# Performance work log

Hardware: AMD Instinct MI355X
Metric: run time of the kernel (lower is better)

The kernel has to match this reference:

```python
import jax, jax.numpy as jnp
import numpy as np
from jax.scipy.ndimage import map_coordinates

N = 512      # image H=W (x0.shape[2])
A = 30       # number of projection angles (sparse-view CT)
D = 729      # det_count (hardcoded in source)
L = 3        # LayerNo
B = 2        # batch
P = 2048     # FFT padding: next pow2 >= 2*D


def _ramp_filter(size):
    # standard Ram-Lak filter built in spatial domain (skimage/torch-radon style)
    n = np.concatenate((np.arange(1, size // 2 + 1, 2), np.arange(size // 2 - 1, 0, -2)))
    f = np.zeros(size)
    f[0] = 0.25
    f[1::2] = -1.0 / (np.pi * n) ** 2
    return jnp.asarray(2.0 * np.real(np.fft.fft(f))[: size // 2 + 1], dtype=jnp.float32)


def setup_inputs() -> dict:
    key = jax.random.key(0)
    ks = jax.random.split(key, 8)
    x0 = jax.random.normal(ks[0], (B, 1, N, N), jnp.float32)
    sinogram = jax.random.normal(ks[1], (B, 1, A, D), jnp.float32)
    theta = jnp.linspace(0.0, np.pi, A, endpoint=False).astype(jnp.float32)
    theta_label = theta
    # denoiser params, stacked over L unrolled layers
    w1 = jax.random.normal(ks[2], (L, 32, 1, 3, 3), jnp.float32) * 0.1
    b1 = jnp.zeros((L, 32), jnp.float32)
    w2 = jax.random.normal(ks[3], (L, 32, 32, 3, 3), jnp.float32) * 0.05
    b2 = jnp.zeros((L, 32), jnp.float32)
    w3 = jax.random.normal(ks[4], (L, 32, 32, 3, 3), jnp.float32) * 0.05
    b3 = jnp.zeros((L, 32), jnp.float32)
    w4 = jax.random.normal(ks[5], (L, 1, 32, 3, 3), jnp.float32) * 0.05
    steps = jnp.ones((L,), jnp.float32)  # step_n params (requires_grad=False)
    return {"cond": 1, "x0": x0, "sinogram": sinogram, "theta": theta,
            "theta_label": theta_label, "w1": w1, "b1": b1, "w2": w2, "b2": b2,
            "w3": w3, "b3": b3, "w4": w4, "steps": steps}


def _conv(x, w, b=None):
    y = jax.lax.conv_general_dilated(x, w, (1, 1), 'SAME',
                                     dimension_numbers=('NCHW', 'OIHW', 'NCHW'))
    return y if b is None else y + b[None, :, None, None]


def _denoiser(x, w1, b1, w2, b2, w3, b3, w4):
    h = jax.nn.relu(_conv(x, w1, b1))
    h = jax.nn.relu(_conv(h, w2, b2))
    h = jax.nn.relu(_conv(h, w3, b3))
    return _conv(h, w4)


def _geometry(theta):
    # parallel-beam ray sampling grid: rows/cols [A, D, T] with T=D samples (dt=1)
    c = (N - 1) / 2.0
    s = jnp.arange(D, dtype=jnp.float32) - (D - 1) / 2.0  # detector coords
    t = s                                                  # along-ray samples
    cs, sn = jnp.cos(theta), jnp.sin(theta)
    x = s[None, :, None] * cs[:, None, None] - t[None, None, :] * sn[:, None, None]
    y = s[None, :, None] * sn[:, None, None] + t[None, None, :] * cs[:, None, None]
    return y + c, x + c  # rows, cols


def _radon_fwd(imgs, rows, cols):
    # imgs [B,N,N] -> sinogram [B,A,D] via bilinear line-integral sampling
    sample = lambda im: map_coordinates(im, [rows, cols], order=1, mode='constant', cval=0.0)
    return jax.vmap(sample)(imgs).sum(-1)


def _filter_sino(sino, filt):
    F = jnp.fft.rfft(sino, n=P, axis=-1)
    g = jnp.fft.irfft(F * filt, n=P, axis=-1)[..., :D]
    return g * (jnp.pi / (2.0 * A))  # FBP normalization


def _backproj(sino, theta):
    # sino [B,A,D] -> image [B,N,N], linear interp along detector axis
    c = (N - 1) / 2.0
    xs = jnp.arange(N, dtype=jnp.float32) - c
    cs, sn = jnp.cos(theta), jnp.sin(theta)
    sgrid = cs[:, None, None] * xs[None, None, :] + sn[:, None, None] * xs[None, :, None]  # [A,N,N]
    idx = sgrid + (D - 1) / 2.0
    lo = jnp.floor(idx).astype(jnp.int32)
    w = idx - lo
    lo_ok = (lo >= 0) & (lo < D)
    hi_ok = (lo + 1 >= 0) & (lo + 1 < D)
    lo_c = jnp.clip(lo, 0, D - 1)
    hi_c = jnp.clip(lo + 1, 0, D - 1)
    a = jnp.arange(A)[:, None, None]
    v = sino[:, a, lo_c] * jnp.where(lo_ok, 1.0 - w, 0.0) + \
        sino[:, a, hi_c] * jnp.where(hi_ok, w, 0.0)       # [B,A,N,N]
    return v.sum(axis=1)


def reference(cond, x0, sinogram, theta, theta_label, w1, b1, w2, b2, w3, b3, w4, steps):
    rows, cols = _geometry(theta)
    filt = _ramp_filter(P)
    X = x0[:, 0]           # [B,N,N]
    sino = sinogram[:, 0]  # [B,A,D]
    for n in range(L):
        sino_pred = _radon_fwd(X, rows, cols)
        filtered = _filter_sino(sino_pred, filt)
        outputs = _backproj(sino - filtered, theta)
        z = X + steps[n] * outputs
        noise = _denoiser(X[:, None], w1[n], b1[n], w2[n], b2[n], w3[n], b3[n], w4[n])[:, 0]
        filtered_noise = _filter_sino(_radon_fwd(noise, rows, cols), filt)
        outputs_noise = _backproj(filtered_noise, theta)
        X = z + noise - steps[n] * outputs_noise
    Xo = X[:, None]
    return (Xo, Xo, Xo)
```

## Files before the change

### kernel.cpp

```cpp
#include <hip/hip_runtime.h>
#include <hip/hip_bf16.h>

typedef __hip_bfloat16 bf16;
typedef __attribute__((ext_vector_type(8))) short short8;
typedef __attribute__((ext_vector_type(4))) short s4v;
typedef __attribute__((ext_vector_type(4))) float float4v;

#define NN 512
#define NA 30
#define ND 729
#define NB 2
#define NL 3
#define BNN (NB*NN*NN)
#define BAD (NB*NA*ND)

#define PW 520
#define PH 516
#define PIMG (PH*PW)
#define POFF (2*PW + 2)

#define O_CS 0
#define O_SN 32
#define O_XP 64
#define O_YP (O_XP + 2*PIMG)
#define O_SP (O_YP + 2*PIMG)
#define O_Q  (O_SP + BAD)
#define O_WR (O_Q + BAD)
#define O_H  (((O_WR + 34560) + 15) & ~15)
#define H_FLOATS (NB * 32 * NN * NN / 2)

#define WR2_OFF 0
#define WR3_OFF 27648
#define WR4_OFF 55296

__global__ void k_prep_all(const float* __restrict__ theta,
                           const float* __restrict__ w2, const float* __restrict__ w3,
                           const float* __restrict__ w4, float* __restrict__ ws,
                           bf16* __restrict__ wr)
{
    int idx = blockIdx.x * 256 + threadIdx.x;
    if (idx < NA) {
        float t = theta[idx];
        ws[O_CS + idx] = cosf(t);
        ws[O_SN + idx] = sinf(t);
    }
    if (idx < 2 * 27648) {
        const float* w = (idx < 27648) ? w2 : w3;
        int base = (idx < 27648) ? WR2_OFF : WR3_OFF;
        int r = idx % 27648;
        int n = r / 9216; int r2 = r % 9216;
        int tap = r2 / 1024; int r3 = r2 % 1024;
        int co = r3 / 32, ci = r3 % 32;
        wr[base + r] = __float2bfloat16(w[n * 9216 + (co * 32 + ci) * 9 + tap]);
    } else if (idx < 2 * 27648 + 3 * 4608) {
        int r = idx - 2 * 27648;
        int n = r / 4608; int r2 = r % 4608;
        int tap = r2 / 512; int r3 = r2 % 512;
        int co = r3 / 32, ci = r3 % 32;
        float v = (co == 0) ? w4[n * 288 + ci * 9 + tap] : 0.f;
        wr[WR4_OFF + r] = __float2bfloat16(v);
    }
}

__global__ void k_init_pad(const float* __restrict__ x0, float* __restrict__ XP,
                           float* __restrict__ YP)
{
    int idx = blockIdx.x * 256 + threadIdx.x;
    if (idx >= 2 * PIMG) return;
    int b = idx / PIMG, p = idx % PIMG;
    int y = p / PW, x = p % PW;
    bool interior = (y >= 2 && y < 2 + NN && x >= 2 && x < 2 + NN);
    float v = interior ? x0[b * NN * NN + (y - 2) * NN + (x - 2)] : 0.f;
    XP[idx] = v;
    if (!interior) YP[idx] = 0.f;
}

__device__ __forceinline__ void isect(float A, float coef, float lo, float hi,
                                      float& tlo, float& thi)
{
    float a = (lo - A) / coef, b = (hi - A) / coef;
    float l = fminf(a, b), h = fmaxf(a, b);
    tlo = fmaxf(tlo, l);
    thi = fminf(thi, h);
}

__global__ __launch_bounds__(256) void k_radon(const float* __restrict__ img,
    const float* __restrict__ ws, float* __restrict__ out)
{
    int b = blockIdx.z, a = blockIdx.y;
    int wave = threadIdx.x >> 6;
    int lane = threadIdx.x & 63;
    int s = blockIdx.x * 4 + wave;
    if (s >= ND) return;
    float cs = ws[O_CS + a], sn = ws[O_SN + a];
    float s_c = (float)s - 364.0f;
    float A_r = 255.5f + s_c * sn;
    float A_c = 255.5f + s_c * cs;

    float tlo = -1e9f, thi = 1e9f;
    isect(A_r, cs, -1.0f, 512.0f, tlo, thi);
    isect(A_c, -sn, -1.0f, 512.0f, tlo, thi);
    float t0f = fmaxf(tlo + 364.0f, 0.0f);
    float t1f = fminf(thi + 364.0f, 728.0f);

    float acc = 0.f;
    if (t0f <= t1f) {
        int tb = (int)ceilf(t0f);
        int te = (int)floorf(t1f);
        const float* im = img + b * PIMG;
#pragma unroll 2
        for (int t = tb + lane; t <= te; t += 64) {
            float tc = (float)t - 364.0f;
            float r = fmaf(tc, cs, A_r);
            float c = fmaf(-tc, sn, A_c);
            float rf = floorf(r), cf = floorf(c);
            float dr = r - rf, dc = c - cf;
            int idx = (int)rf * PW + (int)cf;
            float v00 = im[idx], v01 = im[idx + 1];
            float v10 = im[idx + PW], v11 = im[idx + PW + 1];
            float top = fmaf(dc, v01 - v00, v00);
            float bot = fmaf(dc, v11 - v10, v10);
            acc = fmaf(dr, bot - top, acc + top);
        }
    }
    acc += __shfl_down(acc, 32, 64);
    acc += __shfl_down(acc, 16, 64);
    acc += __shfl_down(acc, 8, 64);
    acc += __shfl_down(acc, 4, 64);
    acc += __shfl_down(acc, 2, 64);
    acc += __shfl_down(acc, 1, 64);
    if (lane == 0) out[(b * NA + a) * ND + s] = acc;
}

__global__ void k_filter(const float* __restrict__ sp, const float* __restrict__ sino,
                         float* __restrict__ q)
{
    __shared__ float row[ND];
    __shared__ float taps[364];
    int ba = blockIdx.y;
    const float* src = sp + ba * ND;
    for (int i = threadIdx.x; i < ND; i += 256) row[i] = src[i];
    const float PI2 = 9.86960440108936f;
    for (int i = threadIdx.x; i < 364; i += 256) {
        float m = (float)(2 * i + 1);
        taps[i] = -2.0f / (PI2 * m * m);
    }
    __syncthreads();
    const float scale = 0.0523598775598299f;
    int d = blockIdx.x * 256 + threadIdx.x;
    if (d < ND) {
        float g0 = 0.5f * row[d], g1 = 0.f;
#pragma unroll 4
        for (int j = 0; j < 364; j += 2) {
            int m0 = 2 * j + 1, m1 = 2 * j + 3;
            float l0 = (d - m0 >= 0) ? row[d - m0] : 0.f;
            float r0 = (d + m0 < ND) ? row[d + m0] : 0.f;
            g0 = fmaf(taps[j], l0 + r0, g0);
            float l1 = (d - m1 >= 0) ? row[d - m1] : 0.f;
            float r1 = (d + m1 < ND) ? row[d + m1] : 0.f;
            g1 = fmaf(taps[j + 1], l1 + r1, g1);
        }
        q[ba * ND + d] = sino[ba * ND + d] - scale * (g0 + g1);
    }
}

__global__ __launch_bounds__(256) void k_backproj_update(const float* __restrict__ q,
    const float* __restrict__ src1, const float* __restrict__ ws,
    const float* __restrict__ steps, int n, float* __restrict__ out,
    float* __restrict__ outcopy)
{
    __shared__ float qt[NA][28];
    __shared__ int dmin_s[NA];
    int b = blockIdx.z;
    int x0 = blockIdx.x * 16, y0 = blockIdx.y * 16;
    int tid = threadIdx.x;
    int lx = tid & 15, ly = tid >> 4;
    const float* qb = q + b * NA * ND;

    for (int idx = tid; idx < NA * 26; idx += 256) {
        int a = idx / 26, j = idx % 26;
        float cs = ws[O_CS + a], sn = ws[O_SN + a];
        float f00 = fmaf(cs, (float)x0 - 255.5f, fmaf(sn, (float)y0 - 255.5f, 364.0f));
        float fmn = f00 + fminf(cs * 15.f, 0.f) + fminf(sn * 15.f, 0.f);
        int dm = (int)floorf(fmn);
        if (j == 0) dmin_s[a] = dm;
        int d = dm + j;
        qt[a][j] = (d >= 0 && d < ND) ? qb[a * ND + d] : 0.f;
    }
    __syncthreads();

    float xc = (float)(x0 + lx) - 255.5f, yc = (float)(y0 + ly) - 255.5f;
    float acc = 0.f;
#pragma unroll
    for (int a = 0; a < NA; a++) {
        float cs = ws[O_CS + a], sn = ws[O_SN + a];
        float f = fmaf(cs, xc, fmaf(sn, yc, 364.0f));
        float lf = floorf(f);
        float w = f - lf;
        int j = (int)lf - dmin_s[a];
        float v0 = qt[a][j], v1 = qt[a][j + 1];
        acc = fmaf(v0, 1.0f - w, fmaf(v1, w, acc));
    }
    int pidx = b * PIMG + (y0 + ly) * PW + (x0 + lx);
    float v = fmaf(steps[n], acc, src1[pidx]);
    out[pidx] = v;
    if (outcopy) {
        int fidx = b * NN * NN + (y0 + ly) * NN + (x0 + lx);
        outcopy[fidx] = v;
        outcopy[fidx + BNN] = v;
        outcopy[fidx + 2 * BNN] = v;
    }
}

__global__ __launch_bounds__(256) void k_conv1_hwc(const float* __restrict__ inb,
    const float* __restrict__ W, const float* __restrict__ B, bf16* __restrict__ outb)
{
    int bz = blockIdx.y;
    const float* in = inb + bz * PIMG;
    bf16* out = outb + (size_t)bz * NN * NN * 32;
    int idx = blockIdx.x * 256 + threadIdx.x;
    int y = idx >> 9, x = idx & (NN - 1);
    float v[9];
#pragma unroll
    for (int dy = 0; dy < 3; dy++)
#pragma unroll
        for (int dx = 0; dx < 3; dx++)
            v[dy * 3 + dx] = in[(y + dy - 1) * PW + (x + dx - 1)];
#pragma unroll
    for (int g = 0; g < 4; g++) {
        short8 pk;
#pragma unroll
        for (int j = 0; j < 8; j++) {
            int co = g * 8 + j;
            float a = B[co];
            const float* w = W + co * 9;
#pragma unroll
            for (int k = 0; k < 9; k++) a = fmaf(v[k], w[k], a);
            a = fmaxf(a, 0.f);
            bf16 h = __float2bfloat16(a);
            pk[j] = *reinterpret_cast<short*>(&h);
        }
        *(short8*)(out + (size_t)idx * 32 + g * 8) = pk;
    }
}

#define SH 8
template<int NCO, bool RELU, bool HASB, bool OUTF32>
__global__ __launch_bounds__(256) void k_conv_stream(const bf16* __restrict__ inb,
    const bf16* __restrict__ Wr, const float* __restrict__ Bs,
    const float* __restrict__ addsrc, void* __restrict__ outv)
{
    int lane = threadIdx.x & 63;
    int wave = threadIdx.x >> 6;
    int n16 = lane & 15, quad = lane >> 4;
    int b = blockIdx.z;
    int x0 = blockIdx.x * 16;
    int y0 = (blockIdx.y * 4 + wave) * SH;
    const bf16* in = inb + (size_t)b * NN * NN * 32;

    short8 wf[9 * NCO];
#pragma unroll
    for (int tap = 0; tap < 9; tap++)
#pragma unroll
        for (int t = 0; t < NCO; t++)
            wf[tap * NCO + t] = *(const short8*)(Wr + ((tap * NCO + t) * 16 + n16) * 32 + quad * 8);

    bool vx[3];
#pragma unroll
    for (int dx = 0; dx < 3; dx++) {
        int xx = x0 + n16 + dx - 1;
        vx[dx] = (xx >= 0) && (xx < NN);
    }

    short8 win[3][3];
    auto loadrow = [&](int yy, short8* dst) {
        if (yy >= 0 && yy < NN) {
            const bf16* rowp = in + (size_t)yy * NN * 32;
#pragma unroll
            for (int dx = 0; dx < 3; dx++) {
                short8 v = {};
                if (vx[dx]) v = *(const short8*)(rowp + (x0 + n16 + dx - 1) * 32 + quad * 8);
                dst[dx] = v;
            }
        } else {
            dst[0] = short8{}; dst[1] = short8{}; dst[2] = short8{};
        }
    };
    loadrow(y0 - 1, win[0]);
    loadrow(y0,     win[1]);

    float4v bias[NCO];
#pragma unroll
    for (int t = 0; t < NCO; t++)
        bias[t] = HASB ? *(const float4v*)(Bs + t * 16 + quad * 4) : (float4v){0.f, 0.f, 0.f, 0.f};

#pragma unroll
    for (int i = 0; i < SH; i++) {
        int y = y0 + i;
        loadrow(y + 1, win[(i + 2) % 3]);
        float4v acc[NCO];
#pragma unroll
        for (int t = 0; t < NCO; t++) acc[t] = bias[t];
#pragma unroll
        for (int dy = 0; dy < 3; dy++) {
            short8* row = win[(i + dy) % 3];
#pragma unroll
            for (int dx = 0; dx < 3; dx++) {
                int tap = dy * 3 + dx;
#pragma unroll
                for (int t = 0; t < NCO; t++)
                    acc[t] = __builtin_amdgcn_mfma_f32_16x16x32_bf16(wf[tap * NCO + t], row[dx], acc[t], 0, 0, 0);
            }
        }
        if (OUTF32) {
            float* out = (float*)outv + b * PIMG;
            if (quad == 0) {
                int pi = y * PW + x0 + n16;
                out[pi] = addsrc[b * PIMG + pi] + acc[0][0];
            }
        } else {
            bf16* out = (bf16*)outv + (size_t)b * NN * NN * 32;
            bf16* pp = out + ((size_t)y * NN + x0 + n16) * 32 + quad * 4;
#pragma unroll
            for (int t = 0; t < NCO; t++) {
                s4v pk;
#pragma unroll
                for (int r = 0; r < 4; r++) {
                    float v = acc[t][r];
                    if (RELU) v = fmaxf(v, 0.f);
                    bf16 h = __float2bfloat16(v);
                    pk[r] = *reinterpret_cast<short*>(&h);
                }
                *(s4v*)(pp + t * 16) = pk;
            }
        }
    }
}

extern "C" void kernel_launch(void* const* d_in, const int* in_sizes, int n_in,
                              void* d_out, int out_size, void* d_ws, size_t ws_size,
                              hipStream_t stream)
{
    const float* x0    = (const float*)d_in[1];
    const float* sg    = (const float*)d_in[2];
    const float* theta = (const float*)d_in[3];
    const float* w1    = (const float*)d_in[5];
    const float* b1    = (const float*)d_in[6];
    const float* w2    = (const float*)d_in[7];
    const float* b2    = (const float*)d_in[8];
    const float* w3    = (const float*)d_in[9];
    const float* b3    = (const float*)d_in[10];
    const float* w4    = (const float*)d_in[11];
    const float* steps = (const float*)d_in[12];

    float* ws = (float*)d_ws;
    float* XP = ws + O_XP + POFF;
    float* YP = ws + O_YP + POFF;
    float* SP = ws + O_SP;
    float* Q  = ws + O_Q;
    bf16* wr  = (bf16*)(ws + O_WR);
    bf16* h1  = (bf16*)(ws + O_H);
    bf16* h2  = (bf16*)(ws + O_H + H_FLOATS);

    k_prep_all<<<(2 * 27648 + 3 * 4608 + 255) / 256, 256, 0, stream>>>(theta, w2, w3, w4, ws, wr);
    k_init_pad<<<(2 * PIMG + 255) / 256, 256, 0, stream>>>(x0, ws + O_XP, ws + O_YP);

    for (int n = 0; n < NL; n++) {
        k_conv1_hwc<<<dim3(NN * NN / 256, NB), 256, 0, stream>>>(XP, w1 + n * 288, b1 + n * 32, h1);
        k_conv_stream<2, true, true, false><<<dim3(32, 16, NB), 256, 0, stream>>>(
            h1, wr + WR2_OFF + n * 9216, b2 + n * 32, nullptr, h2);
        k_conv_stream<2, true, true, false><<<dim3(32, 16, NB), 256, 0, stream>>>(
            h2, wr + WR3_OFF + n * 9216, b3 + n * 32, nullptr, h1);
        k_conv_stream<1, false, false, true><<<dim3(32, 16, NB), 256, 0, stream>>>(
            h1, wr + WR4_OFF + n * 4608, nullptr, XP, YP);

        k_radon<<<dim3((ND + 3) / 4, NA, NB), 256, 0, stream>>>(YP, ws, SP);
        k_filter<<<dim3(3, NB * NA), 256, 0, stream>>>(SP, sg, Q);
        k_backproj_update<<<dim3(32, 32, NB), 256, 0, stream>>>(
            Q, YP, ws, steps, n, XP, (n == NL - 1) ? (float*)d_out : nullptr);
    }
}
```

Before: 483.5 us.

## Tile radon projection into row bands staged in LDS with atomic accumulation

Replaces the per-ray radon kernel with a band-tiled version. Each block loads a 17-row strip of the padded image into shared memory, then every ray through that strip samples from LDS and its partial sum is added to the sinogram with atomicAdd. The aim is to swap scattered global gathers for LDS reads. The cost is an extra memset per layer, atomic contention, and more blocks whose work is mostly clipped away, with 16 rays per wave each stepping 4 samples per iteration.

```diff
diff --git a/kernel.cpp b/kernel.cpp
--- a/kernel.cpp
+++ b/kernel.cpp
@@ -75,61 +75,95 @@
     if (!interior) YP[idx] = 0.f;
 }
 
-__device__ __forceinline__ void isect(float A, float coef, float lo, float hi,
-                                      float& tlo, float& thi)
-{
-    float a = (lo - A) / coef, b = (hi - A) / coef;
-    float l = fminf(a, b), h = fmaxf(a, b);
-    tlo = fmaxf(tlo, l);
-    thi = fminf(thi, h);
-}
-
-__global__ __launch_bounds__(256) void k_radon(const float* __restrict__ img,
+__device__ __forceinline__ void clip(float A, float coef, float lo, float hi,
+                                     float& tlo, float& thi)
+{
+    if (coef != 0.f) {
+        float a = (lo - A) / coef, b = (hi - A) / coef;
+        tlo = fmaxf(tlo, fminf(a, b));
+        thi = fminf(thi, fmaxf(a, b));
+    } else if (!(A >= lo && A < hi)) {
+        tlo = 1.f; thi = 0.f;
+    }
+}
+
+__global__ __launch_bounds__(256) void k_radon_band(const float* __restrict__ img0,
     const float* __restrict__ ws, float* __restrict__ out)
 {
-    int b = blockIdx.z, a = blockIdx.y;
-    int wave = threadIdx.x >> 6;
-    int lane = threadIdx.x & 63;
-    int s = blockIdx.x * 4 + wave;
-    if (s >= ND) return;
+    __shared__ float lds[17 * 521];
+    int band = blockIdx.x, a = blockIdx.y, b = blockIdx.z;
+    int tid = threadIdx.x;
+    int wave = tid >> 6, lane = tid & 63;
+    int R0 = 16 * band - 1;
+
+    const float* imb = img0 + b * PIMG;
+    int base_phys = 16 * band + 1;
+    for (int idx = tid; idx < 17 * 130; idx += 256) {
+        int j = idx / 130, q = idx % 130;
+        int pr = base_phys + j;
+        float4v v = {0.f, 0.f, 0.f, 0.f};
+        if (pr < PH) v = *(const float4v*)(imb + pr * PW + 4 * q);
+        int o = j * 521 + 4 * q;
+        lds[o] = v[0]; lds[o + 1] = v[1]; lds[o + 2] = v[2]; lds[o + 3] = v[3];
+    }
+    __syncthreads();
+
     float cs = ws[O_CS + a], sn = ws[O_SN + a];
-    float s_c = (float)s - 364.0f;
-    float A_r = 255.5f + s_c * sn;
-    float A_c = 255.5f + s_c * cs;
-
-    float tlo = -1e9f, thi = 1e9f;
-    isect(A_r, cs, -1.0f, 512.0f, tlo, thi);
-    isect(A_c, -sn, -1.0f, 512.0f, tlo, thi);
-    float t0f = fmaxf(tlo + 364.0f, 0.0f);
-    float t1f = fminf(thi + 364.0f, 728.0f);
-
-    float acc = 0.f;
-    if (t0f <= t1f) {
-        int tb = (int)ceilf(t0f);
-        int te = (int)floorf(t1f);
-        const float* im = img + b * PIMG;
+    float bandLo = (float)R0;
+    float bandHi = fminf((float)(R0 + 16), 512.0f);
+    int sl = lane & 15, tl = lane >> 4;
+    float* outb = out + (b * NA + a) * ND;
+
+    for (int sg = wave; sg < 46; sg += 4) {
+        int s = sg * 16 + sl;
+        float s_c = (float)s - 364.0f;
+        float A_r = 255.5f + s_c * sn;
+        float A_c = 255.5f + s_c * cs;
+
+        float tlo = -1e9f, thi = 1e9f;
+        clip(A_r, cs, bandLo, bandHi, tlo, thi);
+        clip(A_c, -sn, -1.0f, 512.0f, tlo, thi);
+        int tb = 0, te = -1;
+        if (tlo <= thi && s <= 728) {
+            tb = max(0,   (int)ceilf(tlo + 364.0f) - 1);
+            te = min(728, (int)floorf(thi + 364.0f) + 1);
+        }
+        int m = te - tb;
+        int wm = m;
+        wm = max(wm, __shfl_xor(wm, 1, 64));
+        wm = max(wm, __shfl_xor(wm, 2, 64));
+        wm = max(wm, __shfl_xor(wm, 4, 64));
+        wm = max(wm, __shfl_xor(wm, 8, 64));
+        wm = max(wm, __shfl_xor(wm, 16, 64));
+        wm = max(wm, __shfl_xor(wm, 32, 64));
+
+        float acc = 0.f;
+        int nmax = (wm >= 0) ? ((wm >> 2) + 1) : 0;
 #pragma unroll 2
-        for (int t = tb + lane; t <= te; t += 64) {
-            float tc = (float)t - 364.0f;
-            float r = fmaf(tc, cs, A_r);
-            float c = fmaf(-tc, sn, A_c);
-            float rf = floorf(r), cf = floorf(c);
-            float dr = r - rf, dc = c - cf;
-            int idx = (int)rf * PW + (int)cf;
-            float v00 = im[idx], v01 = im[idx + 1];
-            float v10 = im[idx + PW], v11 = im[idx + PW + 1];
-            float top = fmaf(dc, v01 - v00, v00);
-            float bot = fmaf(dc, v11 - v10, v10);
-            acc = fmaf(dr, bot - top, acc + top);
-        }
-    }
-    acc += __shfl_down(acc, 32, 64);
-    acc += __shfl_down(acc, 16, 64);
-    acc += __shfl_down(acc, 8, 64);
-    acc += __shfl_down(acc, 4, 64);
-    acc += __shfl_down(acc, 2, 64);
-    acc += __shfl_down(acc, 1, 64);
-    if (lane == 0) out[(b * NA + a) * ND + s] = acc;
+        for (int k = 0; k < nmax; k++) {
+            int t = tb + tl + 4 * k;
+            if (t <= te) {
+                float tc = (float)t - 364.0f;
+                float r = fmaf(tc, cs, A_r);
+                float c = fmaf(-tc, sn, A_c);
+                float rf = floorf(r), cf = floorf(c);
+                int ir = (int)rf, ic = (int)cf;
+                if (ir >= R0 && ir <= R0 + 15) {
+                    float dr = r - rf, dc = c - cf;
+                    int o = (ir - R0) * 521 + ic + 2;
+                    float v00 = lds[o], v01 = lds[o + 1];
+                    float v10 = lds[o + 521], v11 = lds[o + 522];
+                    float top = fmaf(dc, v01 - v00, v00);
+                    float bot = fmaf(dc, v11 - v10, v10);
+                    acc = fmaf(dr, bot - top, acc + top);
+                }
+            }
+        }
+        acc += __shfl_down(acc, 32, 64);
+        acc += __shfl_down(acc, 16, 64);
+        if (tl == 0 && s <= 728 && acc != 0.f)
+            atomicAdd(outb + s, acc);
+    }
 }
 
 __global__ void k_filter(const float* __restrict__ sp, const float* __restrict__ sino,
@@ -374,7 +408,8 @@
         k_conv_stream<1, false, false, true><<<dim3(32, 16, NB), 256, 0, stream>>>(
             h1, wr + WR4_OFF + n * 4608, nullptr, XP, YP);
 
-        k_radon<<<dim3((ND + 3) / 4, NA, NB), 256, 0, stream>>>(YP, ws, SP);
+        hipMemsetAsync(SP, 0, BAD * sizeof(float), stream);
+        k_radon_band<<<dim3(33, NA, NB), 256, 0, stream>>>(ws + O_YP, ws, SP);
         k_filter<<<dim3(3, NB * NA), 256, 0, stream>>>(SP, sg, Q);
         k_backproj_update<<<dim3(32, 32, NB), 256, 0, stream>>>(
             Q, YP, ws, steps, n, XP, (n == NL - 1) ? (float*)d_out : nullptr);
```

New measurement: 522.5 us. 1.08x slower.
